# Kernel tuning notes

Measured on AMD Instinct MI355X. Metric: run time of the kernel, lower is better.

## Reference

```python
import jax, jax.numpy as jnp
import numpy as np

D_MODEL = 1024
D_STATE = 16
D_CONV = 4
EXPAND = 2
D_INNER = EXPAND * D_MODEL          # 2048
DT_RANK = (D_MODEL + 15) // 16      # 64 (mamba default 'auto')
B_SZ = 4
SEQ = 2048
EPS = 1e-12


def setup_inputs() -> dict:
    key = jax.random.key(0)
    ks = jax.random.split(key, 12)
    s = 0.02
    n = lambda k, sh: (jax.random.normal(k, sh, jnp.float32) * s)
    A_log = jnp.log(jnp.broadcast_to(
        jnp.arange(1, D_STATE + 1, dtype=jnp.float32), (D_INNER, D_STATE)))
    return {
        "input_tensor": jax.random.normal(ks[0], (B_SZ, SEQ, D_MODEL), jnp.float32),
        "in_proj_w": n(ks[1], (2 * D_INNER, D_MODEL)),
        "conv_w": n(ks[2], (D_INNER, D_CONV)),
        "conv_b": n(ks[3], (D_INNER,)),
        "x_proj_w": n(ks[4], (DT_RANK + 2 * D_STATE, D_INNER)),
        "dt_proj_w": n(ks[5], (D_INNER, DT_RANK)),
        "dt_proj_b": jax.random.uniform(ks[6], (D_INNER,), jnp.float32, -4.0, -2.0),
        "A_log": A_log,
        "D": jnp.ones((D_INNER,), jnp.float32),
        "out_proj_w": n(ks[7], (D_MODEL, D_INNER)),
        "norm_w": jnp.ones((D_MODEL,), jnp.float32),
        "ffn_w1": n(ks[8], (4 * D_MODEL, D_MODEL)),
        "ffn_b1": jnp.zeros((4 * D_MODEL,), jnp.float32),
        "ffn_w2": n(ks[9], (D_MODEL, 4 * D_MODEL)),
        "ffn_b2": jnp.zeros((D_MODEL,), jnp.float32),
        "ffn_norm_w": jnp.ones((D_MODEL,), jnp.float32),
    }


def rmsnorm(x, w, eps=EPS):
    return x * jax.lax.rsqrt(jnp.mean(x * x, axis=-1, keepdims=True) + eps) * w


def causal_dwconv(x, w, b):
    # x: (B, L, D); w: (D, K) depthwise causal conv, output length L
    xc = jnp.swapaxes(x, 1, 2)  # (B, D, L)
    out = jax.lax.conv_general_dilated(
        xc, w[:, None, :], window_strides=(1,),
        padding=[(w.shape[1] - 1, 0)],
        dimension_numbers=("NCH", "OIH", "NCH"),
        feature_group_count=w.shape[0])
    return jnp.swapaxes(out, 1, 2) + b


def selective_scan(u, delta, A, Bm, Cm):
    # u, delta: (B, L, D); Bm, Cm: (B, L, N); A: (D, N)
    def step(h, inp):
        d_t, u_t, b_t, c_t = inp           # (B,D), (B,D), (B,N), (B,N)
        dA = jnp.exp(d_t[..., None] * A)   # (B, D, N)
        h = dA * h + (d_t * u_t)[..., None] * b_t[:, None, :]
        y = jnp.einsum("bdn,bn->bd", h, c_t)
        return h, y
    h0 = jnp.zeros((u.shape[0], u.shape[2], A.shape[1]), u.dtype)
    xs = (jnp.swapaxes(delta, 0, 1), jnp.swapaxes(u, 0, 1),
          jnp.swapaxes(Bm, 0, 1), jnp.swapaxes(Cm, 0, 1))
    _, ys = jax.lax.scan(step, h0, xs)     # ys: (L, B, D)
    return jnp.swapaxes(ys, 0, 1)


def mamba_block(x, in_proj_w, conv_w, conv_b, x_proj_w, dt_proj_w, dt_proj_b,
                A_log, D, out_proj_w):
    xz = x @ in_proj_w.T                    # (B, L, 2*D_INNER)
    u, z = jnp.split(xz, 2, axis=-1)
    u = jax.nn.silu(causal_dwconv(u, conv_w, conv_b))
    x_dbl = u @ x_proj_w.T                  # (B, L, dt_rank + 2*N)
    dt = x_dbl[..., :DT_RANK]
    Bm = x_dbl[..., DT_RANK:DT_RANK + D_STATE]
    Cm = x_dbl[..., DT_RANK + D_STATE:]
    delta = jax.nn.softplus(dt @ dt_proj_w.T + dt_proj_b)
    A = -jnp.exp(A_log)
    y = selective_scan(u, delta, A, Bm, Cm) + u * D
    y = y * jax.nn.silu(z)
    return y @ out_proj_w.T


def reference(input_tensor, in_proj_w, conv_w, conv_b, x_proj_w, dt_proj_w,
              dt_proj_b, A_log, D, out_proj_w, norm_w, ffn_w1, ffn_b1,
              ffn_w2, ffn_b2, ffn_norm_w):
    h = mamba_block(input_tensor, in_proj_w, conv_w, conv_b, x_proj_w,
                    dt_proj_w, dt_proj_b, A_log, D, out_proj_w)
    # num_blocks=2 -> residual; dropout is identity at eval
    h = rmsnorm(h + input_tensor, norm_w)
    ff = jax.nn.gelu(h @ ffn_w1.T + ffn_b1, approximate=False) @ ffn_w2.T + ffn_b2
    return rmsnorm(ff + h, ffn_norm_w)
```

## Files before the change

### kernel.cpp

```cpp
#include <hip/hip_runtime.h>
#include <cstdint>
#include <cstddef>

#define SEQ    2048
#define NB     4
#define DM     1024
#define DI     2048
#define MTOK   (NB*SEQ)
#define NCHUNK 16
#define TCH    128

typedef unsigned short u16;
typedef __attribute__((ext_vector_type(8))) short  short8;
typedef __attribute__((ext_vector_type(4))) float  f32x4;
typedef __attribute__((ext_vector_type(4))) unsigned short us4;

__device__ __forceinline__ float b2f(u16 u){ union{unsigned i; float f;} c; c.i=((unsigned)u)<<16; return c.f; }
__device__ __forceinline__ u16 f2b(float f){
  union{float f; unsigned u;} c; c.f=f;
  unsigned r = c.u + 0x7fffu + ((c.u>>16)&1u);
  return (u16)(r>>16);
}

__device__ __forceinline__ void gload_lds16(const void* g, void* l){
  __builtin_amdgcn_global_load_lds((const __attribute__((address_space(1))) void*)g,
                                   (__attribute__((address_space(3))) void*)l, 16, 0, 0);
}

__global__ __launch_bounds__(256) void cvt_k(const float* __restrict__ in,
                                             u16* __restrict__ out, int n8){
  const int i = blockIdx.x*256 + threadIdx.x;
  if (i >= n8) return;
  const f32x4 a = ((const f32x4*)in)[2*i];
  const f32x4 b = ((const f32x4*)in)[2*i+1];
  short8 r;
  #pragma unroll
  for (int e=0;e<4;e++){ r[e] = (short)f2b(a[e]); r[e+4] = (short)f2b(b[e]); }
  ((short8*)out)[i] = r;
}

__global__ __launch_bounds__(256) void padcvt_k(const float* __restrict__ in,
                                                u16* __restrict__ out){
  const int i = blockIdx.x*256 + threadIdx.x;
  const int row = (i*8) >> 11;
  short8 r;
  if (row < 96){
    const f32x4 a = ((const f32x4*)in)[2*i];
    const f32x4 b = ((const f32x4*)in)[2*i+1];
    #pragma unroll
    for (int e=0;e<4;e++){ r[e] = (short)f2b(a[e]); r[e+4] = (short)f2b(b[e]); }
  } else {
    #pragma unroll
    for (int e=0;e<8;e++) r[e] = 0;
  }
  ((short8*)out)[i] = r;
}

template<int MW, int EPI>
__global__ __launch_bounds__(512, 2) void gemm8(
    const u16* __restrict__ X, int lda,
    const u16* __restrict__ W,
    const float* __restrict__ bias,
    void* __restrict__ Cout,
    int N, int K, int gridX)
{
  constexpr int BM = 128*MW;
  __shared__ __align__(16) u16 As[2][MW][128*64];
  __shared__ __align__(16) u16 Bs[2][2][128*64];

  const int nwg  = gridDim.x;
  const int orig = blockIdx.x;
  const int swz  = (orig & 7)*(nwg >> 3) + (orig >> 3);
  const int bm0  = (swz / gridX) * BM;
  const int bn0  = (swz % gridX) * 256;

  const int tid  = threadIdx.x;
  const int lane = tid & 63;
  const int wv   = tid >> 6;
  const int wm   = wv >> 2;
  const int wn   = wv & 3;

  const int trow = tid >> 3;
  const int sl   = tid & 7;
  const int scol = (sl ^ (trow & 7)) << 3;

  const u16* gA = X + (size_t)bm0*lda + scol;
  const u16* gB = W + (size_t)bn0*K   + scol;
  const int nk = K >> 6;

  auto stageA = [&](int slot, int unit, int tile){
    if (tile < nk){
      const int kt = tile << 6;
      #pragma unroll
      for (int l=0;l<2;l++){
        const int hrow = l*64 + trow;
        gload_lds16(gA + (size_t)(unit*128 + hrow)*lda + kt,
                    &As[slot][unit][hrow*64 + sl*8]);
      }
    }
  };
  auto stageB = [&](int slot, int half, int tile){
    if (tile < nk){
      const int kt = tile << 6;
      #pragma unroll
      for (int l=0;l<2;l++){
        const int hrow = l*64 + trow;
        gload_lds16(gB + (size_t)(half*128 + hrow)*K + kt,
                    &Bs[slot][half][hrow*64 + sl*8]);
      }
    }
  };

  f32x4 acc[4][MW][4];
  #pragma unroll
  for (int p=0;p<4;p++)
    #pragma unroll
    for (int i=0;i<MW;i++)
      #pragma unroll
      for (int j=0;j<4;j++){ f32x4 z={0.f,0.f,0.f,0.f}; acc[p][i][j]=z; }

  const int lrow = lane & 15;
  const int lhi  = lane >> 4;
  const int r7   = lane & 7;

  stageB(0,0,0); stageB(0,1,0);
  stageA(0,0,0); if constexpr (MW==2) stageA(0,1,0);
  stageB(1,0,1); stageB(1,1,1);
  if constexpr (MW==2) stageA(1,0,1);
  if constexpr (MW==2) asm volatile("s_waitcnt vmcnt(6)":::"memory");
  else                 asm volatile("s_waitcnt vmcnt(4)":::"memory");
  __builtin_amdgcn_s_barrier();

  for (int T0 = 0; T0 < nk; T0 += 2) {
    #pragma unroll
    for (int sub = 0; sub < 2; ++sub) {
      const int T = T0 + sub;
      short8 bf[4][2];
      #pragma unroll
      for (int p = 0; p < 4; ++p) {
        if (p == 0) {
          #pragma unroll
          for (int j=0;j<4;j++){
            const int gn = wn*64 + j*16 + lrow;
            const int bh = gn >> 7, br = gn & 127;
            #pragma unroll
            for (int ks=0;ks<2;ks++){
              const int s8 = ((ks<<2)|lhi) ^ r7;
              bf[j][ks] = *(const short8*)&Bs[sub][bh][br*64 + s8*8];
            }
          }
        }
        short8 af[MW][2];
        #pragma unroll
        for (int i=0;i<MW;i++){
          const int gm = (2*p + wm)*(16*MW) + i*16 + lrow;
          const int ah = (MW==2) ? (gm >> 7) : 0;
          const int ar = gm & 127;
          #pragma unroll
          for (int ks=0;ks<2;ks++){
            const int s8 = ((ks<<2)|lhi) ^ r7;
            af[i][ks] = *(const short8*)&As[sub][ah][ar*64 + s8*8];
          }
        }
        if (p == 0)      stageA(sub^1, MW-1, T+1);
        else if (p == 1) stageB(sub, 0, T+2);
        else if (p == 2) stageB(sub, 1, T+2);
        else if constexpr (MW==2) { if (p == 3) stageA(sub, 0, T+2); }
        if (p == 3 && T+1 < nk) {
          if (T+2 < nk) {
            if constexpr (MW==2) asm volatile("s_waitcnt vmcnt(6)":::"memory");
            else                 asm volatile("s_waitcnt vmcnt(4)":::"memory");
          } else {
            asm volatile("s_waitcnt vmcnt(0)":::"memory");
          }
        }
        __builtin_amdgcn_s_barrier();
        asm volatile("s_waitcnt lgkmcnt(0)":::"memory");
        __builtin_amdgcn_s_setprio(1);
        #pragma unroll
        for (int ks=0;ks<2;ks++)
          #pragma unroll
          for (int i=0;i<MW;i++)
            #pragma unroll
            for (int j=0;j<4;j++)
              acc[p][i][j] = __builtin_amdgcn_mfma_f32_16x16x32_bf16(af[i][ks], bf[j][ks], acc[p][i][j], 0, 0, 0);
        __builtin_amdgcn_s_setprio(0);
        __builtin_amdgcn_s_barrier();
      }
    }
  }

  const int r0 = (lane >> 4) << 2;
  #pragma unroll
  for (int p=0;p<4;p++){
    #pragma unroll
    for (int i=0;i<MW;i++){
      #pragma unroll
      for (int j=0;j<4;j++){
        const int col = bn0 + wn*64 + j*16 + lrow;
        float bval = 0.f;
        if constexpr (EPI >= 2) bval = bias[col];
        #pragma unroll
        for (int r=0;r<4;r++){
          const int row = bm0 + (2*p + wm)*(16*MW) + i*16 + r0 + r;
          const float v = acc[p][i][j][r];
          const size_t oid = (size_t)row*N + col;
          if constexpr (EPI == 0) {
            ((u16*)Cout)[oid] = f2b(v);
          } else if constexpr (EPI == 1) {
            ((float*)Cout)[oid] = v;
          } else if constexpr (EPI == 2) {
            float xv = v + bval;
            float sp = (xv > 20.f) ? xv : log1pf(__expf(xv));
            ((u16*)Cout)[oid] = f2b(sp);
          } else if constexpr (EPI == 3) {
            float xv = v + bval;
            float g = 0.5f*xv*(1.f + erff(xv*0.70710678118f));
            ((u16*)Cout)[oid] = f2b(g);
          } else {
            ((float*)Cout)[oid] = v + bval;
          }
        }
      }
    }
  }
}

template<int EPI>
__global__ __launch_bounds__(256) void gemm_bt(
    const u16* __restrict__ X, int lda,
    const u16* __restrict__ W,
    const float* __restrict__ bias,
    void* __restrict__ Cout,
    int M, int N, int K)
{
  __shared__ __align__(16) u16 As[128*64];
  __shared__ __align__(16) u16 Bs[128*64];
  const int tid  = threadIdx.x;
  const int lane = tid & 63;
  const int wv   = tid >> 6;
  const int wr   = wv >> 1, wc = wv & 1;
  const int bm0  = blockIdx.y * 128;
  const int bn0  = blockIdx.x * 128;
  const int r0   = tid >> 3;
  const int c8   = (tid & 7) << 3;

  f32x4 acc[4][4];
  #pragma unroll
  for (int i=0;i<4;i++)
    #pragma unroll
    for (int j=0;j<4;j++){ f32x4 z = {0.f,0.f,0.f,0.f}; acc[i][j] = z; }

  const int lrow = lane & 15;
  const int lko  = (lane >> 4) << 3;

  for (int kt = 0; kt < K; kt += 64) {
    #pragma unroll
    for (int c = 0; c < 4; ++c) {
      const int row = c*32 + r0;
      gload_lds16(X + (size_t)(bm0+row)*lda + kt + c8, &As[row*64 + c8]);
      gload_lds16(W + (size_t)(bn0+row)*K   + kt + c8, &Bs[row*64 + c8]);
    }
    __syncthreads();
    #pragma unroll
    for (int kk = 0; kk < 2; ++kk) {
      short8 af[4], bf[4];
      #pragma unroll
      for (int i=0;i<4;i++) af[i] = *(const short8*)&As[(wr*64 + i*16 + lrow)*64 + kk*32 + lko];
      #pragma unroll
      for (int j=0;j<4;j++) bf[j] = *(const short8*)&Bs[(wc*64 + j*16 + lrow)*64 + kk*32 + lko];
      #pragma unroll
      for (int i=0;i<4;i++)
        #pragma unroll
        for (int j=0;j<4;j++)
          acc[i][j] = __builtin_amdgcn_mfma_f32_16x16x32_bf16(af[i], bf[j], acc[i][j], 0, 0, 0);
    }
    __syncthreads();
  }

  const int rbase = bm0 + wr*64 + ((lane>>4)<<2);
  const int cbase = bn0 + wc*64 + (lane & 15);
  #pragma unroll
  for (int i=0;i<4;i++) {
    #pragma unroll
    for (int j=0;j<4;j++) {
      const int col = cbase + j*16;
      float bval = 0.f;
      if constexpr (EPI >= 2) bval = bias[col];
      #pragma unroll
      for (int r=0;r<4;r++) {
        const int row = rbase + i*16 + r;
        const float v = acc[i][j][r];
        const size_t oid = (size_t)row*N + col;
        if constexpr (EPI == 0) {
          ((u16*)Cout)[oid] = f2b(v);
        } else if constexpr (EPI == 1) {
          ((float*)Cout)[oid] = v;
        } else if constexpr (EPI == 2) {
          float xv = v + bval;
          float sp = (xv > 20.f) ? xv : log1pf(__expf(xv));
          ((u16*)Cout)[oid] = f2b(sp);
        } else if constexpr (EPI == 3) {
          float xv = v + bval;
          float g = 0.5f*xv*(1.f + erff(xv*0.70710678118f));
          ((u16*)Cout)[oid] = f2b(g);
        } else {
          ((float*)Cout)[oid] = v + bval;
        }
      }
    }
  }
}

__global__ __launch_bounds__(256) void conv_silu_k(
    const u16* __restrict__ xz, const float* __restrict__ cw,
    const float* __restrict__ cb, u16* __restrict__ uout)
{
  const int m  = blockIdx.x;
  const int t  = m & (SEQ-1);
  const int d8 = threadIdx.x << 3;
  float w[4][8];
  const float* wp = cw + (size_t)d8*4;
  #pragma unroll
  for (int q=0;q<8;q++){
    f32x4 v = ((const f32x4*)wp)[q];
    #pragma unroll
    for (int e=0;e<4;e++){ int li=q*4+e; w[li&3][li>>2]=v[e]; }
  }
  float acc[8];
  {
    f32x4 b0 = ((const f32x4*)&cb[d8])[0];
    f32x4 b1 = ((const f32x4*)&cb[d8])[1];
    #pragma unroll
    for (int e=0;e<4;e++){ acc[e]=b0[e]; acc[e+4]=b1[e]; }
  }
  #pragma unroll
  for (int j=0;j<4;j++){
    const int tt = t - 3 + j;
    if (tt >= 0){
      short8 v = *(const short8*)&xz[(size_t)(m-3+j)*4096 + d8];
      #pragma unroll
      for (int e=0;e<8;e++) acc[e] = fmaf(b2f((u16)v[e]), w[j][e], acc[e]);
    }
  }
  short8 r;
  #pragma unroll
  for (int e=0;e<8;e++){
    float x = acc[e];
    r[e] = (short)f2b(x / (1.f + __expf(-x)));
  }
  *(short8*)&uout[(size_t)m*2048 + d8] = r;
}

template<int PASS>
__global__ __launch_bounds__(256) void scan_chunk_k(
    u16* __restrict__ dly,
    const u16* __restrict__ ucv,
    const u16* __restrict__ xz,
    const u16* __restrict__ xdbl,
    const float* __restrict__ A_log,
    const float* __restrict__ Dp,
    float* __restrict__ summ)
{
  __shared__ __align__(16) u16 sBC [TCH*32];
  __shared__ __align__(16) u16 sDel[16*256];
  __shared__ __align__(16) u16 sU  [16*256];
  __shared__ __align__(16) u16 sZ  [16*256];

  const int tid   = threadIdx.x;
  const int chgrp = blockIdx.x;
  const int chunk = blockIdx.y;
  const int ch    = chgrp*256 + tid;
  const int b     = ch >> 11;
  const int d     = ch & (DI-1);
  const int t0    = chunk*TCH;
  const int dbase = (chgrp & 7) << 8;

  float A[16];
  #pragma unroll
  for (int n=0;n<16;n++) A[n] = -__expf(A_log[d*16 + n]);

  #pragma unroll
  for (int k=0;k<2;k++){
    const int i = k*256 + tid;
    const int row = i >> 2, q8 = (i & 3) << 3;
    *(short8*)&sBC[row*32 + q8] =
      *(const short8*)&xdbl[((size_t)(b*SEQ) + t0 + row)*128 + 64 + q8];
  }

  float h[16];
  if constexpr (PASS == 1) {
    #pragma unroll
    for (int n=0;n<16;n++) h[n] = 0.f;
  } else {
    #pragma unroll
    for (int n=0;n<16;n++) h[n] = summ[((size_t)(chunk*17 + n))*8192 + ch];
  }
  float S = 0.f;
  float Dd = 0.f;
  if constexpr (PASS == 3) Dd = Dp[d];

  const int srow = tid >> 5;
  const int scol = (tid & 31) << 3;
  const size_t gD = (size_t)(b*SEQ)*DI   + dbase + scol;
  const size_t gZ = (size_t)(b*SEQ)*4096 + 2048 + dbase + scol;

  short8 pD[2], pU[2], pZ[2];
  #pragma unroll
  for (int k=0;k<2;k++){
    const size_t tg = (size_t)(t0 + k*8 + srow);
    pD[k] = *(const short8*)&dly[gD + tg*DI];
    pU[k] = *(const short8*)&ucv[gD + tg*DI];
    if constexpr (PASS == 3) pZ[k] = *(const short8*)&xz[gZ + tg*4096];
  }

  for (int sc = 0; sc < 8; ++sc) {
    __syncthreads();
    #pragma unroll
    for (int k=0;k<2;k++){
      *(short8*)&sDel[(k*8+srow)*256 + scol] = pD[k];
      *(short8*)&sU  [(k*8+srow)*256 + scol] = pU[k];
      if constexpr (PASS == 3) *(short8*)&sZ[(k*8+srow)*256 + scol] = pZ[k];
    }
    if (sc < 7) {
      #pragma unroll
      for (int k=0;k<2;k++){
        const size_t tg = (size_t)(t0 + (sc+1)*16 + k*8 + srow);
        pD[k] = *(const short8*)&dly[gD + tg*DI];
        pU[k] = *(const short8*)&ucv[gD + tg*DI];
        if constexpr (PASS == 3) pZ[k] = *(const short8*)&xz[gZ + tg*4096];
      }
    }
    __syncthreads();

    #pragma unroll 2
    for (int j=0; j<16; ++j){
      const int r = sc*16 + j;
      const float del = b2f(sDel[j*256 + tid]);
      const float u   = b2f(sU  [j*256 + tid]);
      const float du  = del * u;
      if constexpr (PASS == 1) S += del;
      const short8 bv0 = *(const short8*)&sBC[r*32];
      const short8 bv1 = *(const short8*)&sBC[r*32 + 8];
      short8 cv0, cv1;
      if constexpr (PASS == 3){
        cv0 = *(const short8*)&sBC[r*32 + 16];
        cv1 = *(const short8*)&sBC[r*32 + 24];
      }
      float p0=0.f, p1=0.f, p2=0.f, p3=0.f;
      #pragma unroll
      for (int n=0;n<16;++n){
        const float Bn = b2f((u16)(n<8 ? bv0[n] : bv1[n-8]));
        const float eA = __expf(del * A[n]);
        h[n] = fmaf(eA, h[n], du * Bn);
        if constexpr (PASS == 3){
          const float Cn = b2f((u16)(n<8 ? cv0[n] : cv1[n-8]));
          if      ((n&3)==0) p0 = fmaf(h[n], Cn, p0);
          else if ((n&3)==1) p1 = fmaf(h[n], Cn, p1);
          else if ((n&3)==2) p2 = fmaf(h[n], Cn, p2);
          else               p3 = fmaf(h[n], Cn, p3);
        }
      }
      if constexpr (PASS == 3){
        const float p = (p0+p1)+(p2+p3);
        const float z = b2f(sZ[j*256 + tid]);
        float y = fmaf(u, Dd, p);
        y *= z / (1.f + __expf(-z));
        dly[(size_t)(b*SEQ + t0 + r)*DI + d] = f2b(y);
      }
    }
  }

  if constexpr (PASS == 1){
    #pragma unroll
    for (int n=0;n<16;n++) summ[((size_t)(chunk*17 + n))*8192 + ch] = h[n];
    summ[((size_t)(chunk*17 + 16))*8192 + ch] = S;
  }
}

__global__ __launch_bounds__(256) void scan_combine_k(
    float* __restrict__ summ, const float* __restrict__ A_log)
{
  const int ch = blockIdx.x*256 + threadIdx.x;
  const int d  = ch & (DI-1);
  float A[16];
  #pragma unroll
  for (int n=0;n<16;n++) A[n] = -__expf(A_log[d*16 + n]);
  float hi[16];
  #pragma unroll
  for (int n=0;n<16;n++) hi[n] = 0.f;
  for (int c=0; c<NCHUNK; ++c){
    float hf[16]; float Sc = 0.f;
    if (c < NCHUNK-1) {
      #pragma unroll
      for (int n=0;n<16;n++) hf[n] = summ[((size_t)(c*17 + n))*8192 + ch];
      Sc = summ[((size_t)(c*17 + 16))*8192 + ch];
    }
    #pragma unroll
    for (int n=0;n<16;n++) summ[((size_t)(c*17 + n))*8192 + ch] = hi[n];
    if (c < NCHUNK-1) {
      #pragma unroll
      for (int n=0;n<16;n++) hi[n] = fmaf(__expf(A[n]*Sc), hi[n], hf[n]);
    }
  }
}

template<bool RES_BF, bool OUT_BF>
__global__ __launch_bounds__(256) void add_rms_k(
    const float* __restrict__ a, const void* __restrict__ res,
    const float* __restrict__ wgt, void* __restrict__ out)
{
  const int row = blockIdx.x;
  const int tid = threadIdx.x;
  const size_t base = (size_t)row*DM + tid*4;
  const f32x4 av = *(const f32x4*)&a[base];
  const f32x4 wv = *(const f32x4*)&wgt[tid*4];
  float v[4]; float ss = 0.f;
  if constexpr (RES_BF) {
    const us4 rv = *(const us4*)&((const u16*)res)[base];
    #pragma unroll
    for (int j=0;j<4;j++){ v[j] = av[j] + b2f(rv[j]); ss = fmaf(v[j], v[j], ss); }
  } else {
    const f32x4 rv = *(const f32x4*)&((const float*)res)[base];
    #pragma unroll
    for (int j=0;j<4;j++){ v[j] = av[j] + rv[j]; ss = fmaf(v[j], v[j], ss); }
  }
  #pragma unroll
  for (int off=32; off>=1; off>>=1) ss += __shfl_xor(ss, off);
  __shared__ float sred[4];
  if ((tid & 63) == 0) sred[tid>>6] = ss;
  __syncthreads();
  const float tot = sred[0]+sred[1]+sred[2]+sred[3];
  const float rs = rsqrtf(tot * (1.f/1024.f) + 1e-12f);
  if constexpr (OUT_BF) {
    us4 ov;
    #pragma unroll
    for (int j=0;j<4;j++) ov[j] = (unsigned short)f2b(v[j] * rs * wv[j]);
    *(us4*)&((u16*)out)[base] = ov;
  } else {
    f32x4 ov;
    #pragma unroll
    for (int j=0;j<4;j++) ov[j] = v[j] * rs * wv[j];
    *(f32x4*)&((float*)out)[base] = ov;
  }
}

extern "C" void kernel_launch(void* const* d_in, const int* in_sizes, int n_in,
                              void* d_out, int out_size, void* d_ws, size_t ws_size,
                              hipStream_t stream) {
  (void)in_sizes; (void)n_in; (void)out_size; (void)ws_size;
  const float* x_in  = (const float*)d_in[0];
  const float* w_inp = (const float*)d_in[1];
  const float* conv_w= (const float*)d_in[2];
  const float* conv_b= (const float*)d_in[3];
  const float* w_xp  = (const float*)d_in[4];
  const float* w_dt  = (const float*)d_in[5];
  const float* b_dt  = (const float*)d_in[6];
  const float* A_log = (const float*)d_in[7];
  const float* Dp    = (const float*)d_in[8];
  const float* w_out = (const float*)d_in[9];
  const float* norm_w= (const float*)d_in[10];
  const float* w_f1  = (const float*)d_in[11];
  const float* b_f1  = (const float*)d_in[12];
  const float* w_f2  = (const float*)d_in[13];
  const float* b_f2  = (const float*)d_in[14];
  const float* norm2 = (const float*)d_in[15];

  char* ws = (char*)d_ws;
  size_t off = 0;
  auto alloc = [&](size_t bytes){ void* p = ws + off; off += (bytes + 255) & ~255ull; return p; };
  u16*   xz   = (u16*)  alloc((size_t)MTOK*4096*2);
  u16*   ucv  = (u16*)  alloc((size_t)MTOK*2048*2);
  u16*   xdbl = (u16*)  alloc((size_t)MTOK*128*2);
  u16*   dly  = (u16*)  alloc((size_t)MTOK*2048*2);
  float* tmp  = (float*)alloc((size_t)MTOK*1024*4);
  u16*   wA   = (u16*)  alloc((size_t)4096*1024*2);
  u16*   wpad = (u16*)  alloc((size_t)128*2048*2);
  u16*   wdt  = (u16*)  alloc((size_t)2048*64*2);
  u16*   wout = (u16*)  alloc((size_t)1024*2048*2);
  u16*   xbf  = (u16*)tmp;
  float* summ = tmp + (size_t)MTOK*512;
  u16*   hbuf = ucv;

  cvt_k<<<4096, 256, 0, stream>>>(x_in,  xbf, MTOK*DM/8);
  cvt_k<<<2048, 256, 0, stream>>>(w_inp, wA,  (2*DI*DM)/8);
  padcvt_k<<<128, 256, 0, stream>>>(w_xp, wpad);
  cvt_k<<<64,   256, 0, stream>>>(w_dt,  wdt, (DI*64)/8);
  cvt_k<<<1024, 256, 0, stream>>>(w_out, wout,(DM*DI)/8);

  gemm8<2,0><<<512, 512, 0, stream>>>(xbf, 1024, wA, nullptr, xz, 4096, 1024, 16);
  conv_silu_k<<<MTOK, 256, 0, stream>>>(xz, conv_w, conv_b, ucv);
  gemm_bt<0><<<dim3(1,64), 256, 0, stream>>>(ucv, 2048, wpad, nullptr, xdbl, MTOK, 128, 2048);
  gemm_bt<2><<<dim3(16,64), 256, 0, stream>>>(xdbl, 128, wdt, b_dt, dly, MTOK, 2048, 64);
  scan_chunk_k<1><<<dim3(32, NCHUNK-1), 256, 0, stream>>>(dly, ucv, xz, xdbl, A_log, Dp, summ);
  scan_combine_k<<<32, 256, 0, stream>>>(summ, A_log);
  scan_chunk_k<3><<<dim3(32, NCHUNK), 256, 0, stream>>>(dly, ucv, xz, xdbl, A_log, Dp, summ);
  gemm8<1,1><<<256, 512, 0, stream>>>(dly, 2048, wout, nullptr, tmp, 1024, 2048, 4);
  add_rms_k<false,true><<<MTOK, 256, 0, stream>>>(tmp, x_in, norm_w, hbuf);
  cvt_k<<<2048, 256, 0, stream>>>(w_f1, wA, (4*DM*DM)/8);
  gemm8<2,3><<<512, 512, 0, stream>>>(hbuf, 1024, wA, b_f1, xz, 4096, 1024, 16);
  cvt_k<<<2048, 256, 0, stream>>>(w_f2, wA, (4*DM*DM)/8);
  gemm8<1,4><<<256, 512, 0, stream>>>(xz, 4096, wA, b_f2, tmp, 1024, 4096, 4);
  add_rms_k<true,false><<<MTOK, 256, 0, stream>>>(tmp, hbuf, norm2, d_out);
}
```

Baseline: 653.7 us.

## Halve scan chunk length, add thin x_proj GEMM, batch conv over four tokens

```diff
diff --git a/kernel.cpp b/kernel.cpp
--- a/kernel.cpp
+++ b/kernel.cpp
@@ -7,8 +7,8 @@
 #define DM     1024
 #define DI     2048
 #define MTOK   (NB*SEQ)
-#define NCHUNK 16
-#define TCH    128
+#define NCHUNK 32
+#define TCH    64
 
 typedef unsigned short u16;
 typedef __attribute__((ext_vector_type(8))) short  short8;
@@ -312,12 +312,73 @@
   }
 }
 
+__global__ __launch_bounds__(256) void gemm_thin(
+    const u16* __restrict__ X, int lda,
+    const u16* __restrict__ W,
+    u16* __restrict__ Cout, int K)
+{
+  __shared__ __align__(16) u16 As[32*64];
+  __shared__ __align__(16) u16 Bs[128*64];
+  const int tid  = threadIdx.x;
+  const int lane = tid & 63;
+  const int wvq  = tid >> 6;
+  const int bm0  = blockIdx.x * 32;
+  const int srow = tid >> 3;
+  const int c8   = (tid & 7) << 3;
+
+  f32x4 acc[2][2];
+  #pragma unroll
+  for (int i=0;i<2;i++)
+    #pragma unroll
+    for (int j=0;j<2;j++){ f32x4 z={0.f,0.f,0.f,0.f}; acc[i][j]=z; }
+
+  const int lrow = lane & 15;
+  const int lko  = (lane >> 4) << 3;
+
+  for (int kt = 0; kt < K; kt += 64) {
+    gload_lds16(X + (size_t)(bm0+srow)*lda + kt + c8, &As[srow*64 + c8]);
+    #pragma unroll
+    for (int c=0;c<4;c++){
+      const int row = c*32 + srow;
+      gload_lds16(W + (size_t)row*K + kt + c8, &Bs[row*64 + c8]);
+    }
+    __syncthreads();
+    #pragma unroll
+    for (int ks=0;ks<2;ks++){
+      short8 af[2], bf[2];
+      #pragma unroll
+      for (int i=0;i<2;i++) af[i] = *(const short8*)&As[(i*16+lrow)*64 + ks*32 + lko];
+      #pragma unroll
+      for (int j=0;j<2;j++) bf[j] = *(const short8*)&Bs[(wvq*32 + j*16 + lrow)*64 + ks*32 + lko];
+      #pragma unroll
+      for (int i=0;i<2;i++)
+        #pragma unroll
+        for (int j=0;j<2;j++)
+          acc[i][j] = __builtin_amdgcn_mfma_f32_16x16x32_bf16(af[i], bf[j], acc[i][j], 0, 0, 0);
+    }
+    __syncthreads();
+  }
+
+  const int r0 = (lane >> 4) << 2;
+  #pragma unroll
+  for (int i=0;i<2;i++)
+    #pragma unroll
+    for (int j=0;j<2;j++){
+      const int col = wvq*32 + j*16 + lrow;
+      #pragma unroll
+      for (int r=0;r<4;r++){
+        const int row = bm0 + i*16 + r0 + r;
+        Cout[(size_t)row*128 + col] = f2b(acc[i][j][r]);
+      }
+    }
+}
+
 __global__ __launch_bounds__(256) void conv_silu_k(
     const u16* __restrict__ xz, const float* __restrict__ cw,
     const float* __restrict__ cb, u16* __restrict__ uout)
 {
-  const int m  = blockIdx.x;
-  const int t  = m & (SEQ-1);
+  const int m0 = blockIdx.x << 2;
+  const int t0 = m0 & (SEQ-1);
   const int d8 = threadIdx.x << 3;
   float w[4][8];
   const float* wp = cw + (size_t)d8*4;
@@ -327,29 +388,38 @@
     #pragma unroll
     for (int e=0;e<4;e++){ int li=q*4+e; w[li&3][li>>2]=v[e]; }
   }
-  float acc[8];
+  float bias[8];
   {
     f32x4 b0 = ((const f32x4*)&cb[d8])[0];
     f32x4 b1 = ((const f32x4*)&cb[d8])[1];
     #pragma unroll
-    for (int e=0;e<4;e++){ acc[e]=b0[e]; acc[e+4]=b1[e]; }
-  }
-  #pragma unroll
-  for (int j=0;j<4;j++){
-    const int tt = t - 3 + j;
-    if (tt >= 0){
-      short8 v = *(const short8*)&xz[(size_t)(m-3+j)*4096 + d8];
-      #pragma unroll
-      for (int e=0;e<8;e++) acc[e] = fmaf(b2f((u16)v[e]), w[j][e], acc[e]);
-    }
-  }
-  short8 r;
-  #pragma unroll
-  for (int e=0;e<8;e++){
-    float x = acc[e];
-    r[e] = (short)f2b(x / (1.f + __expf(-x)));
-  }
-  *(short8*)&uout[(size_t)m*2048 + d8] = r;
+    for (int e=0;e<4;e++){ bias[e]=b0[e]; bias[e+4]=b1[e]; }
+  }
+  float xv[7][8];
+  #pragma unroll
+  for (int r=0;r<7;r++){
+    const int t = t0 - 3 + r;
+    if (t >= 0){
+      short8 v = *(const short8*)&xz[(size_t)(m0-3+r)*4096 + d8];
+      #pragma unroll
+      for (int e=0;e<8;e++) xv[r][e] = b2f((u16)v[e]);
+    } else {
+      #pragma unroll
+      for (int e=0;e<8;e++) xv[r][e] = 0.f;
+    }
+  }
+  #pragma unroll
+  for (int q=0;q<4;q++){
+    short8 r8;
+    #pragma unroll
+    for (int e=0;e<8;e++){
+      float a = bias[e];
+      #pragma unroll
+      for (int j=0;j<4;j++) a = fmaf(xv[q+j][e], w[j][e], a);
+      r8[e] = (short)f2b(a / (1.f + __expf(-a)));
+    }
+    *(short8*)&uout[(size_t)(m0+q)*2048 + d8] = r8;
+  }
 }
 
 template<int PASS>
@@ -380,10 +450,8 @@
   #pragma unroll
   for (int n=0;n<16;n++) A[n] = -__expf(A_log[d*16 + n]);
 
-  #pragma unroll
-  for (int k=0;k<2;k++){
-    const int i = k*256 + tid;
-    const int row = i >> 2, q8 = (i & 3) << 3;
+  {
+    const int row = tid >> 2, q8 = (tid & 3) << 3;
     *(short8*)&sBC[row*32 + q8] =
       *(const short8*)&xdbl[((size_t)(b*SEQ) + t0 + row)*128 + 64 + q8];
   }
@@ -414,7 +482,7 @@
     if constexpr (PASS == 3) pZ[k] = *(const short8*)&xz[gZ + tg*4096];
   }
 
-  for (int sc = 0; sc < 8; ++sc) {
+  for (int sc = 0; sc < TCH/16; ++sc) {
     __syncthreads();
     #pragma unroll
     for (int k=0;k<2;k++){
@@ -422,7 +490,7 @@
       *(short8*)&sU  [(k*8+srow)*256 + scol] = pU[k];
       if constexpr (PASS == 3) *(short8*)&sZ[(k*8+srow)*256 + scol] = pZ[k];
     }
-    if (sc < 7) {
+    if (sc < TCH/16 - 1) {
       #pragma unroll
       for (int k=0;k<2;k++){
         const size_t tg = (size_t)(t0 + (sc+1)*16 + k*8 + srow);
@@ -579,7 +647,7 @@
   u16*   wdt  = (u16*)  alloc((size_t)2048*64*2);
   u16*   wout = (u16*)  alloc((size_t)1024*2048*2);
   u16*   xbf  = (u16*)tmp;
-  float* summ = tmp + (size_t)MTOK*512;
+  float* summ = tmp;
   u16*   hbuf = ucv;
 
   cvt_k<<<4096, 256, 0, stream>>>(x_in,  xbf, MTOK*DM/8);
@@ -589,8 +657,8 @@
   cvt_k<<<1024, 256, 0, stream>>>(w_out, wout,(DM*DI)/8);
 
   gemm8<2,0><<<512, 512, 0, stream>>>(xbf, 1024, wA, nullptr, xz, 4096, 1024, 16);
-  conv_silu_k<<<MTOK, 256, 0, stream>>>(xz, conv_w, conv_b, ucv);
-  gemm_bt<0><<<dim3(1,64), 256, 0, stream>>>(ucv, 2048, wpad, nullptr, xdbl, MTOK, 128, 2048);
+  conv_silu_k<<<MTOK/4, 256, 0, stream>>>(xz, conv_w, conv_b, ucv);
+  gemm_thin<<<256, 256, 0, stream>>>(ucv, 2048, wpad, xdbl, 2048);
   gemm_bt<2><<<dim3(16,64), 256, 0, stream>>>(xdbl, 128, wdt, b_dt, dly, MTOK, 2048, 64);
   scan_chunk_k<1><<<dim3(32, NCHUNK-1), 256, 0, stream>>>(dly, ucv, xz, xdbl, A_log, Dp, summ);
   scan_combine_k<<<32, 256, 0, stream>>>(summ, A_log);
```

Result: faster. 622.5 us (-4.8%).
